# Performance work log

Hardware: AMD Instinct MI355X
Metric: run time of the kernel (lower is better)

The kernel has to match this reference:

```python
import jax, jax.numpy as jnp
import numpy as np

B, L, D = 2, 2048, 2048        # batch, seqlen, d_model
DIN, N, R, K = 4096, 16, 128, 4  # d_inner, d_state, dt_rank, d_conv


def setup_inputs() -> dict:
    key = jax.random.key(0)
    ks = jax.random.split(key, 9)
    hidden_states = jax.random.normal(ks[0], (B, L, D), dtype=jnp.float32) * 0.02
    in_proj_w = jax.random.normal(ks[1], (2 * DIN, D), dtype=jnp.float32) * (1.0 / np.sqrt(D))
    conv1d_w = jax.random.normal(ks[2], (DIN, K), dtype=jnp.float32) * (1.0 / np.sqrt(DIN))
    x_proj_w = jax.random.normal(ks[3], (R + 2 * N, DIN), dtype=jnp.float32) * (1.0 / np.sqrt(DIN))
    dt_proj_w = jax.random.normal(ks[4], (DIN, R), dtype=jnp.float32) * (1.0 / np.sqrt(R))
    # dt_proj_bias init: inverse-softplus of dt ~ LogUniform(1e-3, 1e-1), as in init_dtprojbias
    dt = jnp.exp(jax.random.uniform(ks[5], (DIN,)) * (np.log(0.1) - np.log(0.001)) + np.log(0.001))
    dt = jnp.clip(dt, 1e-4, None)
    dt_proj_bias = dt + jnp.log(-jnp.expm1(-dt))
    # A_log init: log(arange(1..N)) broadcast over d_inner (init_A)
    A_log = jnp.broadcast_to(jnp.log(jnp.arange(1, N + 1, dtype=jnp.float32)), (DIN, N))
    D_param = jnp.ones((DIN,), dtype=jnp.float32)
    out_proj_w = jax.random.normal(ks[6], (D, DIN), dtype=jnp.float32) * (1.0 / np.sqrt(DIN))
    return {
        "hidden_states": hidden_states, "in_proj_w": in_proj_w, "conv1d_w": conv1d_w,
        "x_proj_w": x_proj_w, "dt_proj_w": dt_proj_w, "dt_proj_bias": dt_proj_bias,
        "A_log": A_log, "D_param": D_param, "out_proj_w": out_proj_w,
    }


def _mamba_forward(hidden_states, in_proj_w, conv1d_w, x_proj_w, dt_proj_w,
                   dt_proj_bias, A_log, D_param, out_proj_w):
    b, l, _ = hidden_states.shape
    # in_proj: (b,l,d_model) -> (b,l,2*d_inner), split into x and gate z
    xz = jnp.einsum("bld,ed->ble", hidden_states, in_proj_w)
    x, z = jnp.split(xz, 2, axis=-1)  # each (b,l,d_inner)

    # depthwise causal conv1d along l, no bias, then SiLU
    xp = jnp.pad(x, ((0, 0), (K - 1, 0), (0, 0)))
    xc = sum(conv1d_w[:, k] * xp[:, k:k + l, :] for k in range(K))  # (b,l,d_inner)
    xc = jax.nn.silu(xc)

    # x_proj -> dt_rank + 2*d_state, split into dt, B, C
    x_dbl = jnp.einsum("bld,ed->ble", xc, x_proj_w)
    dt_r = x_dbl[..., :R]                    # (b,l,R)
    Bc = x_dbl[..., R:R + N]                 # (b,l,N)
    Cc = x_dbl[..., R + N:]                  # (b,l,N)
    delta = jax.nn.softplus(jnp.einsum("blr,dr->bld", dt_r, dt_proj_w) + dt_proj_bias)  # (b,l,d_inner)

    A = -jnp.exp(A_log)  # (d_inner, N)

    # selective scan: h_t = exp(delta_t*A)*h_{t-1} + delta_t*x_t*B_t; y_t = <h_t, C_t>
    def step(h, inp):
        delta_t, B_t, C_t, x_t = inp  # (b,d), (b,n), (b,n), (b,d)
        dA = jnp.exp(delta_t[..., None] * A)                 # (b,d,n)
        h = h * dA + (delta_t * x_t)[..., None] * B_t[:, None, :]
        y_t = jnp.einsum("bdn,bn->bd", h, C_t)
        return h, y_t

    inputs = (jnp.swapaxes(delta, 0, 1), jnp.swapaxes(Bc, 0, 1),
              jnp.swapaxes(Cc, 0, 1), jnp.swapaxes(xc, 0, 1))
    h0 = jnp.zeros((b, DIN, N), dtype=xc.dtype)
    _, y = jax.lax.scan(step, h0, inputs)     # y: (l,b,d_inner)
    y = jnp.swapaxes(y, 0, 1)                 # (b,l,d_inner)

    y = y + xc * D_param                      # skip term
    y = y * jax.nn.silu(z)                    # gating
    return jnp.einsum("bld,ed->ble", y, out_proj_w)  # (b,l,d_model)


def reference(hidden_states, in_proj_w, conv1d_w, x_proj_w, dt_proj_w,
              dt_proj_bias, A_log, D_param, out_proj_w):
    return _mamba_forward(hidden_states, in_proj_w, conv1d_w, x_proj_w, dt_proj_w,
                          dt_proj_bias, A_log, D_param, out_proj_w)
```

## Files before the change

kernel.cpp:

```cpp
#include <hip/hip_runtime.h>
#include <math.h>

#define DIN   4096
#define NST   16
#define RR    128
#define LSEQ  2048
#define NTOK  4096
#define BB    2
#define CHUNK 64
#define NCH   (LSEQ / CHUNK)
#define KSPL  8
#define KC    (DIN / KSPL)

typedef __attribute__((ext_vector_type(8))) short short8;
typedef __attribute__((ext_vector_type(4))) float f32x4;

__device__ __forceinline__ float sigmoidf_(float x) { return 1.f / (1.f + __expf(-x)); }
__device__ __forceinline__ float softplusf_(float x) {
    return fmaxf(x, 0.f) + log1pf(__expf(-fabsf(x)));
}
__device__ __forceinline__ unsigned short f2bf_(float f) {
    unsigned u = __float_as_uint(f);
    return (unsigned short)((u + 0x7FFFu + ((u >> 16) & 1u)) >> 16);
}
__device__ __forceinline__ void gld_lds16_(const unsigned short* g, unsigned short* l) {
    __builtin_amdgcn_global_load_lds((const __attribute__((address_space(1))) unsigned int*)g,
                                     (__attribute__((address_space(3))) unsigned int*)l,
                                     16, 0, 0);
}

__global__ __launch_bounds__(256)
void f2bf_kernel(const float* __restrict__ src, unsigned short* __restrict__ dst, int n8)
{
    int i = blockIdx.x * 256 + threadIdx.x;
    if (i >= n8) return;
    const float4* s = (const float4*)src + 2 * (size_t)i;
    float4 a = s[0], b = s[1];
    union { unsigned short u[8]; uint4 v; } o;
    o.u[0] = f2bf_(a.x); o.u[1] = f2bf_(a.y); o.u[2] = f2bf_(a.z); o.u[3] = f2bf_(a.w);
    o.u[4] = f2bf_(b.x); o.u[5] = f2bf_(b.y); o.u[6] = f2bf_(b.z); o.u[7] = f2bf_(b.w);
    ((uint4*)dst)[i] = o.v;
}

__global__ __launch_bounds__(256)
void add_f4_kernel(float* __restrict__ dst, const float* __restrict__ src, int n4)
{
    int i = blockIdx.x * 256 + threadIdx.x;
    if (i >= n4) return;
    float4 a = ((const float4*)dst)[i];
    float4 b = ((const float4*)src)[i];
    a.x += b.x; a.y += b.y; a.z += b.z; a.w += b.w;
    ((float4*)dst)[i] = a;
}


#define BAR()        asm volatile("s_barrier" ::: "memory")
#define WAIT_LGKM0() asm volatile("s_waitcnt lgkmcnt(0)" ::: "memory")
#define WAIT_VM(n)   asm volatile("s_waitcnt vmcnt(" #n ")" ::: "memory")


#define RD_A(P, mh) do { _Pragma("unroll") \
  for (int ii = 0; ii < 4; ++ii) { \
      aF[ii][0] = *(const short8*)((P) + (mh)*8192 + ii*2048 + co0); \
      aF[ii][1] = *(const short8*)((P) + (mh)*8192 + ii*2048 + co1); } } while (0)

#define RD_B(P, nh, DST) do { _Pragma("unroll") \
  for (int jj = 0; jj < 2; ++jj) { \
      DST[jj][0] = *(const short8*)((P) + (nh)*4096 + jj*2048 + co0); \
      DST[jj][1] = *(const short8*)((P) + (nh)*4096 + jj*2048 + co1); } } while (0)

#define MFMA_Q(mh, nh, BF) do { __builtin_amdgcn_s_setprio(1); _Pragma("unroll") \
  for (int ii = 0; ii < 4; ++ii) { _Pragma("unroll") \
    for (int jj = 0; jj < 2; ++jj) { _Pragma("unroll") \
      for (int ks = 0; ks < 2; ++ks) \
        acc[(mh)*4+ii][(nh)*2+jj] = __builtin_amdgcn_mfma_f32_16x16x32_bf16( \
            aF[ii][ks], BF[jj][ks], acc[(mh)*4+ii][(nh)*2+jj], 0, 0, 0); } } \
  __builtin_amdgcn_s_setprio(0); } while (0)

#define STGLD(gbase, sbase, h, l, tile) \
  gld_lds16_(gbase + (size_t)((h)*128 + (l)*64) * K + (size_t)(tile)*64, \
             (unsigned short*)(sbase + (h)*16384 + (l)*8192))

#define ITER(t, PREF) do { \
   \
  RD_A(pA0, 0); RD_B(pB0c, 0, bA); RD_B(pB0c, 1, bB); \
  STGLD(gA0, sA1, 1, 0, (t)+1); STGLD(gA0, sA1, 1, 1, (t)+1); \
  BAR(); WAIT_LGKM0(); MFMA_Q(0, 0, bA); MFMA_Q(0, 1, bB); BAR(); \
   \
  RD_A(pA0, 1); \
  if (PREF) { STGLD(gA0, sA0, 0, 0, (t)+2); STGLD(gA0, sA0, 0, 1, (t)+2); \
              STGLD(gB0, sB0, 0, 0, (t)+2); STGLD(gB0, sB0, 0, 1, (t)+2); \
              STGLD(gB0, sB0, 1, 0, (t)+2); STGLD(gB0, sB0, 1, 1, (t)+2); } \
  BAR(); WAIT_LGKM0(); MFMA_Q(1, 1, bB); MFMA_Q(1, 0, bA); \
  if (PREF) { WAIT_VM(6); } else { WAIT_VM(0); } \
  BAR(); \
   \
  RD_A(pA1, 0); RD_B(pB1c, 0, bA); RD_B(pB1c, 1, bB); \
  if (PREF) { STGLD(gA0, sA0, 1, 0, (t)+2); STGLD(gA0, sA0, 1, 1, (t)+2); } \
  BAR(); WAIT_LGKM0(); MFMA_Q(0, 0, bA); MFMA_Q(0, 1, bB); BAR(); \
   \
  RD_A(pA1, 1); \
  if (PREF) { STGLD(gA0, sA1, 0, 0, (t)+3); STGLD(gA0, sA1, 0, 1, (t)+3); \
              STGLD(gB0, sB1, 0, 0, (t)+3); STGLD(gB0, sB1, 0, 1, (t)+3); \
              STGLD(gB0, sB1, 1, 0, (t)+3); STGLD(gB0, sB1, 1, 1, (t)+3); } \
  BAR(); WAIT_LGKM0(); MFMA_Q(1, 1, bB); MFMA_Q(1, 0, bA); \
  if (PREF) { WAIT_VM(6); } else { WAIT_VM(0); } \
  BAR(); \
} while (0)

template<int MODE>
__global__ __launch_bounds__(512)
void gemm256(const unsigned short* __restrict__ A, const unsigned short* __restrict__ W,
             float* __restrict__ C, int K, int KL, int ldc, float* __restrict__ C2,
             int nbx, int fx)
{
    __shared__ __align__(16) unsigned short sm[65536];
    char* smb = (char*)sm;

    const int tid = threadIdx.x;
    const int ln  = tid & 63;
    const int wv  = tid >> 6;
    const int wm  = wv >> 2;
    const int wn  = wv & 3;
    const int m15 = ln & 15;
    const int q   = ln >> 4;

    const int bid = blockIdx.x;
    const int xcd = bid & 7;
    const int idx = bid >> 3;
    const int cw  = nbx / fx;
    const int chh = (gridDim.x >> 3) / cw;
    const int bn_i = (xcd % fx) * cw  + idx % cw;
    int bm_i = (xcd / fx) * chh + idx / cw;
    int kh = 0;
    if (MODE == 3) { kh = bm_i >> 4; bm_i &= 15; }
    const int bm  = bm_i << 8;
    const int bn  = bn_i << 8;

    const int co0 = (q * 16) ^ ((m15 & 7) << 4);
    const int co1 = co0 ^ 64;
    const int ra_base = wm * 16384 + m15 * 128;
    const int rb_base = wn * 8192  + m15 * 128;
    const char* pA0  = smb + ra_base;
    const char* pA1  = smb + 65536 + ra_base;
    const char* pB0c = smb + 32768 + rb_base;
    const char* pB1c = smb + 98304 + rb_base;

    char* sA0 = smb +          tid * 16;
    char* sB0 = smb + 32768  + tid * 16;
    char* sA1 = smb + 65536  + tid * 16;
    char* sB1 = smb + 98304  + tid * 16;
    const int srow  = tid >> 3;
    const int secol = (((tid & 7) ^ ((tid >> 3) & 7)) * 8);
    const unsigned short* gA0 = A + (size_t)(bm + srow) * K + secol + (size_t)kh * KL;
    const unsigned short* gB0 = W + (size_t)(bn + srow) * K + secol + (size_t)kh * KL;

    f32x4  acc[8][4] = {};
    short8 aF[4][2], bA[2][2], bB[2][2];

    const int KT = KL >> 6;

    STGLD(gA0, sA0, 0, 0, 0); STGLD(gA0, sA0, 0, 1, 0);
    STGLD(gA0, sA0, 1, 0, 0); STGLD(gA0, sA0, 1, 1, 0);
    STGLD(gB0, sB0, 0, 0, 0); STGLD(gB0, sB0, 0, 1, 0);
    STGLD(gB0, sB0, 1, 0, 0); STGLD(gB0, sB0, 1, 1, 0);
    STGLD(gA0, sA1, 0, 0, 1); STGLD(gA0, sA1, 0, 1, 1);
    STGLD(gB0, sB1, 0, 0, 1); STGLD(gB0, sB1, 0, 1, 1);
    STGLD(gB0, sB1, 1, 0, 1); STGLD(gB0, sB1, 1, 1, 1);
    WAIT_VM(6);
    BAR();

    for (int t = 0; t < KT - 2; t += 2) ITER(t, 1);
    ITER(KT - 2, 0);

    float* Cp = C;
    int bcol = bn;
    if (MODE == 2 && bcol >= DIN) { Cp = C2; bcol -= DIN; }
    if (MODE == 3 && kh) Cp = C2;
    #pragma unroll
    for (int i = 0; i < 8; ++i) {
        int row = bm + wm * 128 + i * 16 + q * 4;
        #pragma unroll
        for (int j = 0; j < 4; ++j) {
            int col = bcol + wn * 64 + j * 16 + m15;
            #pragma unroll
            for (int r = 0; r < 4; ++r)
                Cp[(size_t)(row + r) * ldc + col] = acc[i][j][r];
        }
    }
}

template<int MODE>
__global__ __launch_bounds__(256)
void gemm_mfma_bt(const unsigned short* __restrict__ A, const unsigned short* __restrict__ W,
                  float* __restrict__ C, int K, int ldc,
                  const float* __restrict__ bias, float* __restrict__ C2)
{
    __shared__ unsigned short As[128 * 32];
    __shared__ unsigned short Ws[128 * 32];
    const int tid = threadIdx.x;
    const int bm = blockIdx.y << 7;
    int bn = blockIdx.x << 7;

    const int c0 = tid, c1 = tid + 256;
    const unsigned short* ga0 = A + (size_t)(bm + (c0 >> 2)) * K + (c0 & 3) * 8;
    const unsigned short* ga1 = A + (size_t)(bm + (c1 >> 2)) * K + (c1 & 3) * 8;
    const unsigned short* gw0 = W + (size_t)(bn + (c0 >> 2)) * K + (c0 & 3) * 8;
    const unsigned short* gw1 = W + (size_t)(bn + (c1 >> 2)) * K + (c1 & 3) * 8;
    unsigned short* la0 = &As[c0 * 8];
    unsigned short* la1 = &As[c1 * 8];
    unsigned short* lw0 = &Ws[c0 * 8];
    unsigned short* lw1 = &Ws[c1 * 8];

    const int ln  = tid & 63;
    const int wv  = tid >> 6;
    const int wm  = (wv >> 1) << 6;
    const int wn  = (wv & 1) << 6;
    const int m15 = ln & 15;
    const int q   = ln >> 4;

    f32x4 acc[4][4] = {};

    for (int k0 = 0; k0 < K; k0 += 32) {
        __syncthreads();
        gld_lds16_(ga0, la0); gld_lds16_(ga1, la1);
        gld_lds16_(gw0, lw0); gld_lds16_(gw1, lw1);
        ga0 += 32; ga1 += 32; gw0 += 32; gw1 += 32;
        __syncthreads();
        short8 af[4], wf[4];
        #pragma unroll
        for (int i = 0; i < 4; ++i)
            af[i] = *(const short8*)&As[(wm + i * 16 + m15) * 32 + q * 8];
        #pragma unroll
        for (int j = 0; j < 4; ++j)
            wf[j] = *(const short8*)&Ws[(wn + j * 16 + m15) * 32 + q * 8];
        #pragma unroll
        for (int i = 0; i < 4; ++i)
            #pragma unroll
            for (int j = 0; j < 4; ++j)
                acc[i][j] = __builtin_amdgcn_mfma_f32_16x16x32_bf16(af[i], wf[j],
                                                                    acc[i][j], 0, 0, 0);
    }

    float* Cp = C;
    if (MODE == 2 && bn >= DIN) { Cp = C2; bn -= DIN; }

    #pragma unroll
    for (int i = 0; i < 4; ++i)
        #pragma unroll
        for (int j = 0; j < 4; ++j) {
            int col = bn + wn + j * 16 + m15;
            #pragma unroll
            for (int r = 0; r < 4; ++r) {
                int row = bm + wm + i * 16 + q * 4 + r;
                float v = acc[i][j][r];
                if (MODE == 1) v = softplusf_(v + bias[col]);
                Cp[(size_t)row * ldc + col] = v;
            }
        }
}

__global__ __launch_bounds__(256)
void gemm_kspl_kernel(const float* __restrict__ A, const float* __restrict__ W,
                      float* __restrict__ partial)
{
    __shared__ float As[16][66];
    __shared__ float Ws[16][162];
    const int tid = threadIdx.x;
    const int tx = tid & 15;
    const int ty = tid >> 4;
    const int bm = blockIdx.x << 6;
    const int k0 = blockIdx.y * KC;

    float acc[4][10] = {};

    for (int kt = 0; kt < KC; kt += 16) {
        float2 a2[2];
        #pragma unroll
        for (int i = 0; i < 2; ++i) {
            int idx = tid + 256 * i;
            int row = idx >> 3, kofs = (idx & 7) * 2;
            a2[i] = *(const float2*)&A[(size_t)(bm + row) * DIN + k0 + kt + kofs];
        }
        float2 w2[5];
        #pragma unroll
        for (int i = 0; i < 5; ++i) {
            int idx = tid + 256 * i;
            int wrow = idx >> 3, wk = (idx & 7) * 2;
            w2[i] = *(const float2*)&W[(size_t)wrow * DIN + k0 + kt + wk];
        }
        __syncthreads();
        #pragma unroll
        for (int i = 0; i < 2; ++i) {
            int idx = tid + 256 * i;
            int row = idx >> 3, kofs = (idx & 7) * 2;
            As[kofs][row] = a2[i].x; As[kofs + 1][row] = a2[i].y;
        }
        #pragma unroll
        for (int i = 0; i < 5; ++i) {
            int idx = tid + 256 * i;
            int wrow = idx >> 3, wk = (idx & 7) * 2;
            Ws[wk][wrow] = w2[i].x; Ws[wk + 1][wrow] = w2[i].y;
        }
        __syncthreads();
        #pragma unroll
        for (int kk = 0; kk < 16; ++kk) {
            float2 av0 = *(const float2*)&As[kk][ty * 4];
            float2 av1 = *(const float2*)&As[kk][ty * 4 + 2];
            float a[4] = {av0.x, av0.y, av1.x, av1.y};
            float w[10];
            #pragma unroll
            for (int j = 0; j < 5; ++j) {
                float2 wv = *(const float2*)&Ws[kk][tx * 10 + 2 * j];
                w[2 * j] = wv.x; w[2 * j + 1] = wv.y;
            }
            #pragma unroll
            for (int i = 0; i < 4; ++i)
                #pragma unroll
                for (int j = 0; j < 10; ++j)
                    acc[i][j] = fmaf(a[i], w[j], acc[i][j]);
        }
        __syncthreads();
    }

    float* po = partial + (size_t)blockIdx.y * NTOK * 160;
    #pragma unroll
    for (int i = 0; i < 4; ++i) {
        int r = bm + ty * 4 + i;
        #pragma unroll
        for (int j = 0; j < 5; ++j)
            *(float2*)&po[(size_t)r * 160 + tx * 10 + 2 * j] =
                make_float2(acc[i][2 * j], acc[i][2 * j + 1]);
    }
}

__global__ __launch_bounds__(256)
void kspl_reduce_kernel(const float* __restrict__ partial, float* __restrict__ xdbl,
                        unsigned short* __restrict__ dtr)
{
    int idx = blockIdx.x * 256 + threadIdx.x;
    float s = 0.f;
    #pragma unroll
    for (int k = 0; k < KSPL; ++k)
        s += partial[(size_t)k * NTOK * 160 + idx];
    xdbl[idx] = s;
    int row = idx / 160;
    int col = idx - row * 160;
    if (col < RR) dtr[(size_t)row * RR + col] = f2bf_(s);
}

__global__ __launch_bounds__(256)
void conv_silu_kernel(const float* __restrict__ x, const float* __restrict__ cw,
                      float* __restrict__ xc)
{
    int idx = blockIdx.x * 256 + threadIdx.x;
    int d = idx & (DIN - 1);
    int tok = idx >> 12;
    int t = tok & (LSEQ - 1);
    float w0 = cw[d * 4 + 0], w1 = cw[d * 4 + 1];
    float w2 = cw[d * 4 + 2], w3 = cw[d * 4 + 3];
    const float* xp = x + (size_t)tok * DIN + d;
    float acc = w3 * xp[0];
    if (t >= 1) acc = fmaf(w2, xp[-DIN], acc);
    if (t >= 2) acc = fmaf(w1, xp[-2 * DIN], acc);
    if (t >= 3) acc = fmaf(w0, xp[-3 * DIN], acc);
    xc[idx] = acc * sigmoidf_(acc);
}

__global__ __launch_bounds__(256)
void scan_part1_kernel(const float* __restrict__ delta, const float* __restrict__ xc,
                       const float* __restrict__ xdbl, const float* __restrict__ A_log,
                       float* __restrict__ hloc, float* __restrict__ ssum)
{
    int d = blockIdx.x * 256 + threadIdx.x;
    int c = blockIdx.y;
    int b = blockIdx.z;
    float A[NST], h[NST];
    #pragma unroll
    for (int n = 0; n < NST; ++n) {
        A[n] = -__expf(A_log[d * NST + n]);
        h[n] = 0.f;
    }
    float s = 0.f;
    int tok = b * LSEQ + c * CHUNK;
    for (int t = 0; t < CHUNK; ++t, ++tok) {
        float dv = delta[(size_t)tok * DIN + d];
        float xv = xc[(size_t)tok * DIN + d];
        const float* bc = xdbl + (size_t)tok * 160 + RR;
        float dx = dv * xv;
        s += dv;
        #pragma unroll
        for (int n = 0; n < NST; ++n)
            h[n] = fmaf(h[n], __expf(dv * A[n]), dx * bc[n]);
    }
    size_t base = (size_t)(b * NCH + c) * NST * DIN + d;
    #pragma unroll
    for (int n = 0; n < NST; ++n) hloc[base + (size_t)n * DIN] = h[n];
    ssum[(size_t)(b * NCH + c) * DIN + d] = s;
}

__global__ __launch_bounds__(256)
void scan_part2_kernel(float* __restrict__ hloc, const float* __restrict__ ssum,
                       const float* __restrict__ A_log)
{
    int idx = blockIdx.x * 256 + threadIdx.x;
    int b = idx >> 12;
    int d = idx & (DIN - 1);
    float A[NST], hin[NST];
    #pragma unroll
    for (int n = 0; n < NST; ++n) {
        A[n] = -__expf(A_log[d * NST + n]);
        hin[n] = 0.f;
    }
    for (int c = 0; c < NCH; ++c) {
        size_t base = (size_t)(b * NCH + c) * NST * DIN + d;
        float s = ssum[(size_t)(b * NCH + c) * DIN + d];
        #pragma unroll
        for (int n = 0; n < NST; ++n) {
            float hl = hloc[base + (size_t)n * DIN];
            hloc[base + (size_t)n * DIN] = hin[n];
            hin[n] = fmaf(hin[n], __expf(A[n] * s), hl);
        }
    }
}

__global__ __launch_bounds__(256)
void scan_part3_kernel(const float* __restrict__ delta, float* __restrict__ xcy,
                       const float* __restrict__ xdbl, const float* __restrict__ z,
                       const float* __restrict__ A_log, const float* __restrict__ Dp,
                       const float* __restrict__ hin_buf)
{
    int d = blockIdx.x * 256 + threadIdx.x;
    int c = blockIdx.y;
    int b = blockIdx.z;
    float A[NST], h[NST];
    size_t base = (size_t)(b * NCH + c) * NST * DIN + d;
    #pragma unroll
    for (int n = 0; n < NST; ++n) {
        A[n] = -__expf(A_log[d * NST + n]);
        h[n] = hin_buf[base + (size_t)n * DIN];
    }
    float Dv = Dp[d];
    int tok = b * LSEQ + c * CHUNK;
    for (int t = 0; t < CHUNK; ++t, ++tok) {
        float dv = delta[(size_t)tok * DIN + d];
        float xv = xcy[(size_t)tok * DIN + d];
        float zv = z[(size_t)tok * DIN + d];
        const float* bc = xdbl + (size_t)tok * 160 + RR;
        float dx = dv * xv;
        float y = 0.f;
        #pragma unroll
        for (int n = 0; n < NST; ++n) {
            h[n] = fmaf(h[n], __expf(dv * A[n]), dx * bc[n]);
            y = fmaf(h[n], bc[NST + n], y);
        }
        y = (y + xv * Dv) * (zv * sigmoidf_(zv));
        xcy[(size_t)tok * DIN + d] = y;
    }
}

extern "C" void kernel_launch(void* const* d_in, const int* in_sizes, int n_in,
                              void* d_out, int out_size, void* d_ws, size_t ws_size,
                              hipStream_t stream)
{
    const float* hidden     = (const float*)d_in[0];
    const float* in_proj_w  = (const float*)d_in[1];
    const float* conv_w     = (const float*)d_in[2];
    const float* x_proj_w   = (const float*)d_in[3];
    const float* dt_proj_w  = (const float*)d_in[4];
    const float* dt_bias    = (const float*)d_in[5];
    const float* A_log      = (const float*)d_in[6];
    const float* D_param    = (const float*)d_in[7];
    const float* out_proj_w = (const float*)d_in[8];
    float* out = (float*)d_out;

    const size_t BIG = (size_t)NTOK * DIN * sizeof(float);
    char* ws = (char*)d_ws;
    float* xbuf = (float*)(ws);
    float* xc   = (float*)(ws + BIG);
    float* zbuf = (float*)(ws + 2 * BIG);
    float* xdbl = (float*)(ws + 3 * BIG);
    float* delta = xbuf;

    unsigned short* w_in_bf  = (unsigned short*)xc;
    unsigned short* hid_bf   = (unsigned short*)out;
    unsigned short* y_bf     = (unsigned short*)xbuf;
    unsigned short* w_out_bf = (unsigned short*)zbuf;

    float* xpart = out;
    unsigned short* dtr_bf = (unsigned short*)(out + (size_t)KSPL * NTOK * 160);
    unsigned short* dtw_bf = dtr_bf + (size_t)NTOK * RR;
    float* hloc  = out;
    float* ssum  = out + (size_t)BB * NCH * NST * DIN;

    f2bf_kernel<<<8192, 256, 0, stream>>>(in_proj_w, w_in_bf, (2 * DIN * 2048) / 8);
    f2bf_kernel<<<4096, 256, 0, stream>>>(hidden, hid_bf, (NTOK * 2048) / 8);
    gemm256<2><<<512, 512, 0, stream>>>(hid_bf, w_in_bf, xbuf, 2048, 2048, DIN,
                                        zbuf, 32, 4);
    conv_silu_kernel<<<(NTOK * DIN) / 256, 256, 0, stream>>>(xbuf, conv_w, xc);
    gemm_kspl_kernel<<<dim3(NTOK / 64, KSPL), 256, 0, stream>>>(xc, x_proj_w, xpart);
    kspl_reduce_kernel<<<(NTOK * 160) / 256, 256, 0, stream>>>(xpart, xdbl, dtr_bf);
    f2bf_kernel<<<256, 256, 0, stream>>>(dt_proj_w, dtw_bf, (DIN * RR) / 8);
    gemm_mfma_bt<1><<<dim3(32, 32), 256, 0, stream>>>(dtr_bf, dtw_bf, delta,
                                                      RR, DIN, dt_bias, nullptr);
    scan_part1_kernel<<<dim3(DIN / 256, NCH, BB), 256, 0, stream>>>(delta, xc, xdbl,
                                                                    A_log, hloc, ssum);
    scan_part2_kernel<<<(BB * DIN) / 256, 256, 0, stream>>>(hloc, ssum, A_log);
    scan_part3_kernel<<<dim3(DIN / 256, NCH, BB), 256, 0, stream>>>(delta, xc, xdbl,
                                                                    zbuf, A_log, D_param, hloc);
    f2bf_kernel<<<8192, 256, 0, stream>>>(xc, y_bf, (NTOK * DIN) / 8);
    f2bf_kernel<<<4096, 256, 0, stream>>>(out_proj_w, w_out_bf, (2048 * DIN) / 8);
    gemm256<3><<<256, 512, 0, stream>>>(y_bf, w_out_bf, out, 4096, 2048, 2048,
                                        xc, 8, 2);
    add_f4_kernel<<<8192, 256, 0, stream>>>(out, xc, (NTOK * 2048) / 4);
}
```

Before: 717.8 us.

## Replace 256x256 GEMM tile with 128x128 tile for in/out projections

The 512-thread 256x256-tile GEMM becomes a 256-thread 128x128-tile GEMM with half the LDS, used for both the in_proj and out_proj matmuls. Grid sizes and the XCD swizzle parameters are rescaled to match. The global-to-LDS prefetch is simplified: the whole next K tile is staged at once with a full vmcnt(0) wait each half-iteration, replacing the earlier partial staggered waits. Smaller tiles give more blocks and better occupancy per CU, at the cost of lower arithmetic intensity per tile and less overlap of loads with MFMA work.

```diff
diff --git a/kernel.cpp b/kernel.cpp
--- a/kernel.cpp
+++ b/kernel.cpp
@@ -59,69 +59,78 @@
 #define WAIT_VM(n)   asm volatile("s_waitcnt vmcnt(" #n ")" ::: "memory")
 
 
-#define RD_A(P, mh) do { _Pragma("unroll") \
+#define RD_A8(P) do { _Pragma("unroll") \
   for (int ii = 0; ii < 4; ++ii) { \
-      aF[ii][0] = *(const short8*)((P) + (mh)*8192 + ii*2048 + co0); \
-      aF[ii][1] = *(const short8*)((P) + (mh)*8192 + ii*2048 + co1); } } while (0)
-
-#define RD_B(P, nh, DST) do { _Pragma("unroll") \
+      aF[ii][0] = *(const short8*)((P) + ii*2048 + co0); \
+      aF[ii][1] = *(const short8*)((P) + ii*2048 + co1); } } while (0)
+
+#define RD_B01(P) do { _Pragma("unroll") \
   for (int jj = 0; jj < 2; ++jj) { \
-      DST[jj][0] = *(const short8*)((P) + (nh)*4096 + jj*2048 + co0); \
-      DST[jj][1] = *(const short8*)((P) + (nh)*4096 + jj*2048 + co1); } } while (0)
-
-#define MFMA_Q(mh, nh, BF) do { __builtin_amdgcn_s_setprio(1); _Pragma("unroll") \
+      bA[jj][0] = *(const short8*)((P) + jj*2048 + co0); \
+      bA[jj][1] = *(const short8*)((P) + jj*2048 + co1); } } while (0)
+
+#define RD_B23(P) do { _Pragma("unroll") \
+  for (int jj = 0; jj < 2; ++jj) { \
+      bB[jj][0] = *(const short8*)((P) + 4096 + jj*2048 + co0); \
+      bB[jj][1] = *(const short8*)((P) + 4096 + jj*2048 + co1); } } while (0)
+
+#define MFMA_N01() do { __builtin_amdgcn_s_setprio(1); _Pragma("unroll") \
   for (int ii = 0; ii < 4; ++ii) { _Pragma("unroll") \
     for (int jj = 0; jj < 2; ++jj) { _Pragma("unroll") \
       for (int ks = 0; ks < 2; ++ks) \
-        acc[(mh)*4+ii][(nh)*2+jj] = __builtin_amdgcn_mfma_f32_16x16x32_bf16( \
-            aF[ii][ks], BF[jj][ks], acc[(mh)*4+ii][(nh)*2+jj], 0, 0, 0); } } \
+        acc[ii][jj] = __builtin_amdgcn_mfma_f32_16x16x32_bf16( \
+            aF[ii][ks], bA[jj][ks], acc[ii][jj], 0, 0, 0); } } \
   __builtin_amdgcn_s_setprio(0); } while (0)
 
-#define STGLD(gbase, sbase, h, l, tile) \
-  gld_lds16_(gbase + (size_t)((h)*128 + (l)*64) * K + (size_t)(tile)*64, \
-             (unsigned short*)(sbase + (h)*16384 + (l)*8192))
-
-#define ITER(t, PREF) do { \
+#define MFMA_N23() do { __builtin_amdgcn_s_setprio(1); _Pragma("unroll") \
+  for (int ii = 0; ii < 4; ++ii) { _Pragma("unroll") \
+    for (int jj = 0; jj < 2; ++jj) { _Pragma("unroll") \
+      for (int ks = 0; ks < 2; ++ks) \
+        acc[ii][2+jj] = __builtin_amdgcn_mfma_f32_16x16x32_bf16( \
+            aF[ii][ks], bB[jj][ks], acc[ii][2+jj], 0, 0, 0); } } \
+  __builtin_amdgcn_s_setprio(0); } while (0)
+
+#define STG(gbase, sbase, h, tile) \
+  gld_lds16_(gbase + (size_t)((h)*32) * K + (size_t)(tile)*64, \
+             (unsigned short*)((sbase) + (h)*4096))
+
+#define STG_ALL(gA, sA, gB, sB, tile) do { \
+  STG(gA, sA, 0, tile); STG(gA, sA, 1, tile); \
+  STG(gA, sA, 2, tile); STG(gA, sA, 3, tile); \
+  STG(gB, sB, 0, tile); STG(gB, sB, 1, tile); \
+  STG(gB, sB, 2, tile); STG(gB, sB, 3, tile); } while (0)
+
+#define ITER128(t, PREF) do { \
    \
-  RD_A(pA0, 0); RD_B(pB0c, 0, bA); RD_B(pB0c, 1, bB); \
-  STGLD(gA0, sA1, 1, 0, (t)+1); STGLD(gA0, sA1, 1, 1, (t)+1); \
-  BAR(); WAIT_LGKM0(); MFMA_Q(0, 0, bA); MFMA_Q(0, 1, bB); BAR(); \
+  STG_ALL(gA0, sA1, gB0, sB1, (t)+1); \
+  RD_A8(pA0); RD_B01(pB0); \
+  BAR(); WAIT_LGKM0(); MFMA_N01(); BAR(); \
    \
-  RD_A(pA0, 1); \
-  if (PREF) { STGLD(gA0, sA0, 0, 0, (t)+2); STGLD(gA0, sA0, 0, 1, (t)+2); \
-              STGLD(gB0, sB0, 0, 0, (t)+2); STGLD(gB0, sB0, 0, 1, (t)+2); \
-              STGLD(gB0, sB0, 1, 0, (t)+2); STGLD(gB0, sB0, 1, 1, (t)+2); } \
-  BAR(); WAIT_LGKM0(); MFMA_Q(1, 1, bB); MFMA_Q(1, 0, bA); \
-  if (PREF) { WAIT_VM(6); } else { WAIT_VM(0); } \
-  BAR(); \
+  RD_B23(pB0); \
+  BAR(); WAIT_LGKM0(); MFMA_N23(); WAIT_VM(0); BAR(); \
    \
-  RD_A(pA1, 0); RD_B(pB1c, 0, bA); RD_B(pB1c, 1, bB); \
-  if (PREF) { STGLD(gA0, sA0, 1, 0, (t)+2); STGLD(gA0, sA0, 1, 1, (t)+2); } \
-  BAR(); WAIT_LGKM0(); MFMA_Q(0, 0, bA); MFMA_Q(0, 1, bB); BAR(); \
+  if (PREF) { STG_ALL(gA0, sA0, gB0, sB0, (t)+2); } \
+  RD_A8(pA1); RD_B01(pB1); \
+  BAR(); WAIT_LGKM0(); MFMA_N01(); BAR(); \
    \
-  RD_A(pA1, 1); \
-  if (PREF) { STGLD(gA0, sA1, 0, 0, (t)+3); STGLD(gA0, sA1, 0, 1, (t)+3); \
-              STGLD(gB0, sB1, 0, 0, (t)+3); STGLD(gB0, sB1, 0, 1, (t)+3); \
-              STGLD(gB0, sB1, 1, 0, (t)+3); STGLD(gB0, sB1, 1, 1, (t)+3); } \
-  BAR(); WAIT_LGKM0(); MFMA_Q(1, 1, bB); MFMA_Q(1, 0, bA); \
-  if (PREF) { WAIT_VM(6); } else { WAIT_VM(0); } \
-  BAR(); \
+  RD_B23(pB1); \
+  BAR(); WAIT_LGKM0(); MFMA_N23(); WAIT_VM(0); BAR(); \
 } while (0)
 
 template<int MODE>
-__global__ __launch_bounds__(512)
-void gemm256(const unsigned short* __restrict__ A, const unsigned short* __restrict__ W,
+__global__ __launch_bounds__(256)
+void gemm128(const unsigned short* __restrict__ A, const unsigned short* __restrict__ W,
              float* __restrict__ C, int K, int KL, int ldc, float* __restrict__ C2,
              int nbx, int fx)
 {
-    __shared__ __align__(16) unsigned short sm[65536];
+    __shared__ __align__(16) unsigned short sm[32768];
     char* smb = (char*)sm;
 
     const int tid = threadIdx.x;
     const int ln  = tid & 63;
     const int wv  = tid >> 6;
-    const int wm  = wv >> 2;
-    const int wn  = wv & 3;
+    const int wm  = wv >> 1;
+    const int wn  = wv & 1;
     const int m15 = ln & 15;
     const int q   = ln >> 4;
 
@@ -133,53 +142,47 @@
     const int bn_i = (xcd % fx) * cw  + idx % cw;
     int bm_i = (xcd / fx) * chh + idx / cw;
     int kh = 0;
-    if (MODE == 3) { kh = bm_i >> 4; bm_i &= 15; }
-    const int bm  = bm_i << 8;
-    const int bn  = bn_i << 8;
+    if (MODE == 3) { kh = bm_i >> 5; bm_i &= 31; }
+    const int bm  = bm_i << 7;
+    const int bn  = bn_i << 7;
 
     const int co0 = (q * 16) ^ ((m15 & 7) << 4);
     const int co1 = co0 ^ 64;
-    const int ra_base = wm * 16384 + m15 * 128;
-    const int rb_base = wn * 8192  + m15 * 128;
-    const char* pA0  = smb + ra_base;
-    const char* pA1  = smb + 65536 + ra_base;
-    const char* pB0c = smb + 32768 + rb_base;
-    const char* pB1c = smb + 98304 + rb_base;
+    const int ra_base = wm * 8192 + m15 * 128;
+    const int rb_base = wn * 8192 + m15 * 128;
+    const char* pA0 = smb +          ra_base;
+    const char* pB0 = smb + 16384  + rb_base;
+    const char* pA1 = smb + 32768  + ra_base;
+    const char* pB1 = smb + 49152  + rb_base;
 
     char* sA0 = smb +          tid * 16;
-    char* sB0 = smb + 32768  + tid * 16;
-    char* sA1 = smb + 65536  + tid * 16;
-    char* sB1 = smb + 98304  + tid * 16;
+    char* sB0 = smb + 16384  + tid * 16;
+    char* sA1 = smb + 32768  + tid * 16;
+    char* sB1 = smb + 49152  + tid * 16;
     const int srow  = tid >> 3;
     const int secol = (((tid & 7) ^ ((tid >> 3) & 7)) * 8);
     const unsigned short* gA0 = A + (size_t)(bm + srow) * K + secol + (size_t)kh * KL;
     const unsigned short* gB0 = W + (size_t)(bn + srow) * K + secol + (size_t)kh * KL;
 
-    f32x4  acc[8][4] = {};
+    f32x4  acc[4][4] = {};
     short8 aF[4][2], bA[2][2], bB[2][2];
 
     const int KT = KL >> 6;
 
-    STGLD(gA0, sA0, 0, 0, 0); STGLD(gA0, sA0, 0, 1, 0);
-    STGLD(gA0, sA0, 1, 0, 0); STGLD(gA0, sA0, 1, 1, 0);
-    STGLD(gB0, sB0, 0, 0, 0); STGLD(gB0, sB0, 0, 1, 0);
-    STGLD(gB0, sB0, 1, 0, 0); STGLD(gB0, sB0, 1, 1, 0);
-    STGLD(gA0, sA1, 0, 0, 1); STGLD(gA0, sA1, 0, 1, 1);
-    STGLD(gB0, sB1, 0, 0, 1); STGLD(gB0, sB1, 0, 1, 1);
-    STGLD(gB0, sB1, 1, 0, 1); STGLD(gB0, sB1, 1, 1, 1);
-    WAIT_VM(6);
+    STG_ALL(gA0, sA0, gB0, sB0, 0);
+    WAIT_VM(0);
     BAR();
 
-    for (int t = 0; t < KT - 2; t += 2) ITER(t, 1);
-    ITER(KT - 2, 0);
+    for (int t = 0; t < KT - 2; t += 2) ITER128(t, 1);
+    ITER128(KT - 2, 0);
 
     float* Cp = C;
     int bcol = bn;
     if (MODE == 2 && bcol >= DIN) { Cp = C2; bcol -= DIN; }
     if (MODE == 3 && kh) Cp = C2;
     #pragma unroll
-    for (int i = 0; i < 8; ++i) {
-        int row = bm + wm * 128 + i * 16 + q * 4;
+    for (int i = 0; i < 4; ++i) {
+        int row = bm + wm * 64 + i * 16 + q * 4;
         #pragma unroll
         for (int j = 0; j < 4; ++j) {
             int col = bcol + wn * 64 + j * 16 + m15;
@@ -495,8 +498,8 @@
 
     f2bf_kernel<<<8192, 256, 0, stream>>>(in_proj_w, w_in_bf, (2 * DIN * 2048) / 8);
     f2bf_kernel<<<4096, 256, 0, stream>>>(hidden, hid_bf, (NTOK * 2048) / 8);
-    gemm256<2><<<512, 512, 0, stream>>>(hid_bf, w_in_bf, xbuf, 2048, 2048, DIN,
-                                        zbuf, 32, 4);
+    gemm128<2><<<2048, 256, 0, stream>>>(hid_bf, w_in_bf, xbuf, 2048, 2048, DIN,
+                                         zbuf, 64, 4);
     conv_silu_kernel<<<(NTOK * DIN) / 256, 256, 0, stream>>>(xbuf, conv_w, xc);
     gemm_kspl_kernel<<<dim3(NTOK / 64, KSPL), 256, 0, stream>>>(xc, x_proj_w, xpart);
     kspl_reduce_kernel<<<(NTOK * 160) / 256, 256, 0, stream>>>(xpart, xdbl, dtr_bf);
@@ -510,7 +513,7 @@
                                                                     zbuf, A_log, D_param, hloc);
     f2bf_kernel<<<8192, 256, 0, stream>>>(xc, y_bf, (NTOK * DIN) / 8);
     f2bf_kernel<<<4096, 256, 0, stream>>>(out_proj_w, w_out_bf, (2048 * DIN) / 8);
-    gemm256<3><<<256, 512, 0, stream>>>(y_bf, w_out_bf, out, 4096, 2048, 2048,
-                                        xc, 8, 2);
+    gemm128<3><<<1024, 256, 0, stream>>>(y_bf, w_out_bf, out, 4096, 2048, 2048,
+                                         xc, 16, 2);
     add_f4_kernel<<<8192, 256, 0, stream>>>(out, xc, (NTOK * 2048) / 4);
 }
```

After: 756.8 us. 5.4% more time.
